# Performance work log

Hardware: AMD Instinct MI355X
Metric: run time of the kernel (lower is better)

Reference implementation:

```python
import jax, jax.numpy as jnp
import numpy as np

BN_EPS = 1e-5


def setup_inputs() -> dict:
    key = jax.random.key(0)
    ks = jax.random.split(key, 16)
    N, E, IN, H, A, L = 50000, 400000, 128, 192, 192, 3
    s = 0.02
    inp = {
        "x": jax.random.normal(ks[0], (N, IN), dtype=jnp.float32),
        "edge_index": jax.random.randint(ks[1], (2, E), 0, N, dtype=jnp.int32),
        "seed_idx": 123,
        "proj_w": jax.random.normal(ks[2], (IN, H), dtype=jnp.float32) * s,
        "proj_b": jnp.zeros((H,), dtype=jnp.float32),
        "mlp1_w": jax.random.normal(ks[3], (L, H, H), dtype=jnp.float32) * s,
        "mlp1_b": jnp.zeros((L, H), dtype=jnp.float32),
        "mlp2_w": jax.random.normal(ks[4], (L, H, H), dtype=jnp.float32) * s,
        "mlp2_b": jnp.zeros((L, H), dtype=jnp.float32),
        "eps": jnp.zeros((L,), dtype=jnp.float32),  # GIN train_eps init 0
        "bn_g": jnp.ones((L, H), dtype=jnp.float32),
        "bn_b": jnp.zeros((L, H), dtype=jnp.float32),
        "W1": jax.random.normal(ks[5], (H, A), dtype=jnp.float32) * s,
        "W2": jax.random.normal(ks[6], (H, A), dtype=jnp.float32) * s,
        "w_attn": jax.random.normal(ks[7], (A,), dtype=jnp.float32) * s,
        "cls_w": jax.random.normal(ks[8], (H,), dtype=jnp.float32) * s,
        "cls_b": jnp.zeros((1,), dtype=jnp.float32),
    }
    return inp


def _forward(x, edge_index, seed_idx, proj_w, proj_b, mlp1_w, mlp1_b,
             mlp2_w, mlp2_b, eps, bn_g, bn_b, W1, W2, w_attn, cls_w, cls_b):
    N = x.shape[0]
    src, dst = edge_index[0], edge_index[1]
    h = jax.nn.relu(x @ proj_w + proj_b)  # [N, H]
    L = mlp1_w.shape[0]
    for l in range(L):
        # GINConv: mlp((1+eps)*h + sum_{j->i} h_j) via scatter-add on dst
        agg = jax.ops.segment_sum(h[src], dst, num_segments=N)  # [N, H]
        z = (1.0 + eps[l]) * h + agg
        z = jax.nn.relu(z @ mlp1_w[l] + mlp1_b[l]) @ mlp2_w[l] + mlp2_b[l]
        # BatchNorm over nodes (batch statistics)
        mu = z.mean(axis=0)
        var = z.var(axis=0)
        z = (z - mu) * jax.lax.rsqrt(var + BN_EPS) * bn_g[l] + bn_b[l]
        h = jax.nn.relu(z)  # dropout is identity in eval
    h_seed = h[seed_idx]  # valid seed index branch
    zat = jnp.tanh(h @ W1 + h_seed @ W2)          # [N, A]
    e = jax.nn.leaky_relu(zat @ w_attn, 0.2)      # [N]
    alpha = jax.nn.softmax(e, axis=0)             # [N]
    readout = alpha @ h                           # [H]
    logit = readout @ cls_w + cls_b               # [1]
    return logit, alpha


def reference(x, edge_index, seed_idx, proj_w, proj_b, mlp1_w, mlp1_b,
              mlp2_w, mlp2_b, eps, bn_g, bn_b, W1, W2, w_attn, cls_w, cls_b):
    return _forward(x, edge_index, seed_idx, proj_w, proj_b, mlp1_w, mlp1_b,
                    mlp2_w, mlp2_b, eps, bn_g, bn_b, W1, W2, w_attn, cls_w, cls_b)
```

## Files before the change

kernel.cpp:

```cpp
#include <hip/hip_runtime.h>
#include <hip/hip_bf16.h>

#define N_NODES 50000
#define N_EDGES 400000
#define DIM_IN  128
#define DIM_H   192
#define N_LAYERS 3
#define BN_EPSF 1e-5f
#define SCAN_NBLK 49
#define INV_N (1.f / N_NODES)
#define NSHADOW 8
#define SSTRIDE 384

typedef __attribute__((ext_vector_type(8))) short short8;
typedef __attribute__((ext_vector_type(4))) float floatx4;

union FragU { uint4 u; short8 s; };

__device__ __forceinline__ float relu_f(float x) { return x > 0.f ? x : 0.f; }
__device__ __forceinline__ unsigned short f2bf(float x) {
  __hip_bfloat16 h = __float2bfloat16(x);
  return *reinterpret_cast<unsigned short*>(&h);
}
__device__ __forceinline__ float bf2f(unsigned short b) {
  return __uint_as_float(((unsigned)b) << 16);
}
__device__ __forceinline__ float bflo(unsigned u) { return __uint_as_float(u << 16); }
__device__ __forceinline__ float bfhi(unsigned u) { return __uint_as_float(u & 0xffff0000u); }

__global__ void k_hist(const int* __restrict__ edge, int* __restrict__ cnt) {
  int e = blockIdx.x * 256 + threadIdx.x;
  if (e < N_EDGES) atomicAdd(&cnt[edge[N_EDGES + e]], 1);
}

__global__ void k_scanA(const int* __restrict__ deg, int* __restrict__ part, int* __restrict__ bsum) {
  __shared__ int buf[1024];
  int g = blockIdx.x * 1024 + threadIdx.x;
  int v = (g < N_NODES) ? deg[g] : 0;
  buf[threadIdx.x] = v;
  __syncthreads();
  for (int off = 1; off < 1024; off <<= 1) {
    int t = (threadIdx.x >= off) ? buf[threadIdx.x - off] : 0;
    __syncthreads();
    buf[threadIdx.x] += t;
    __syncthreads();
  }
  if (g < N_NODES) part[g] = buf[threadIdx.x];
  if (threadIdx.x == 1023) bsum[blockIdx.x] = buf[1023];
}

__global__ void k_scanB(int* __restrict__ bsum) {
  __shared__ int b[64];
  int t = threadIdx.x;
  b[t] = (t < SCAN_NBLK) ? bsum[t] : 0;
  __syncthreads();
  for (int off = 1; off < 64; off <<= 1) {
    int v = (t >= off) ? b[t - off] : 0;
    __syncthreads();
    b[t] += v;
    __syncthreads();
  }
  if (t < SCAN_NBLK) bsum[t] = t ? b[t - 1] : 0;
}

__global__ void k_scanC(const int* __restrict__ part, const int* __restrict__ bsum,
                        int* __restrict__ rowptr, int* __restrict__ cursor) {
  int g = blockIdx.x * 256 + threadIdx.x;
  if (g == 0) { rowptr[0] = 0; cursor[0] = 0; }
  if (g < N_NODES) {
    int v = part[g] + bsum[g >> 10];
    rowptr[g + 1] = v;
    if (g + 1 < N_NODES) cursor[g + 1] = v;
  }
}

__global__ void k_fill(const int* __restrict__ edge, int* __restrict__ cursor, int* __restrict__ csr) {
  int e = blockIdx.x * 256 + threadIdx.x;
  if (e < N_EDGES) {
    int s = edge[e];
    int d = edge[N_EDGES + e];
    int pos = atomicAdd(&cursor[d], 1);
    csr[pos] = s;
  }
}

__global__ void k_wtp(const float* __restrict__ m1, const float* __restrict__ m2,
                      const float* __restrict__ wa, const float* __restrict__ pw,
                      uint4* __restrict__ outp) {
  const int NH = 7 * 24 * 192;
  const int NP = 16 * 192;
  int idx = blockIdx.x * 256 + threadIdx.x;
  if (idx >= NH + NP) return;
  union { uint4 u; unsigned short h[8]; } fr;
  if (idx < NH) {
    int mat = idx / (24 * 192);
    int rem = idx - mat * (24 * 192);
    int kidx = rem / 192, col = rem - kidx * 192;
    const float* src = mat < 3 ? m1 + (size_t)mat * (DIM_H * DIM_H)
                     : (mat < 6 ? m2 + (size_t)(mat - 3) * (DIM_H * DIM_H) : wa);
#pragma unroll
    for (int t = 0; t < 8; ++t) fr.h[t] = f2bf(src[(size_t)(kidx * 8 + t) * DIM_H + col]);
  } else {
    int rem = idx - NH;
    int kidx = rem / 192, col = rem - kidx * 192;
#pragma unroll
    for (int t = 0; t < 8; ++t) fr.h[t] = f2bf(pw[(size_t)(kidx * 8 + t) * DIM_H + col]);
  }
  outp[idx] = fr.u;
}

template <bool BN>
__global__ void k_agg(const unsigned short* __restrict__ z, const int* __restrict__ rowptr,
                      const int* __restrict__ csr, const float* __restrict__ stats,
                      const float* __restrict__ bng, const float* __restrict__ bnb,
                      const float* __restrict__ eps, int l, unsigned short* __restrict__ outA) {
  int wid = threadIdx.x >> 6, lane = threadIdx.x & 63;
  int node = blockIdx.x * 4 + wid;
  if (node >= N_NODES || lane >= 48) return;
  int c = lane * 4;
  float4 sc4 = {1.f, 1.f, 1.f, 1.f}, sh4 = {0.f, 0.f, 0.f, 0.f};
  if (BN) {
    float4 st = {0.f, 0.f, 0.f, 0.f}, sq = {0.f, 0.f, 0.f, 0.f};
#pragma unroll
    for (int g = 0; g < NSHADOW; ++g) {
      const float* sp = stats + g * SSTRIDE;
      float4 a = *(const float4*)(sp + c);
      float4 b = *(const float4*)(sp + DIM_H + c);
      st.x += a.x; st.y += a.y; st.z += a.z; st.w += a.w;
      sq.x += b.x; sq.y += b.y; sq.z += b.z; sq.w += b.w;
    }
    float4 g4 = *(const float4*)(bng + c);
    float4 b4 = *(const float4*)(bnb + c);
    float mu, rs;
    mu = st.x * INV_N; rs = rsqrtf(sq.x * INV_N - mu * mu + BN_EPSF); sc4.x = g4.x * rs; sh4.x = b4.x - mu * sc4.x;
    mu = st.y * INV_N; rs = rsqrtf(sq.y * INV_N - mu * mu + BN_EPSF); sc4.y = g4.y * rs; sh4.y = b4.y - mu * sc4.y;
    mu = st.z * INV_N; rs = rsqrtf(sq.z * INV_N - mu * mu + BN_EPSF); sc4.z = g4.z * rs; sh4.z = b4.z - mu * sc4.z;
    mu = st.w * INV_N; rs = rsqrtf(sq.w * INV_N - mu * mu + BN_EPSF); sc4.w = g4.w * rs; sh4.w = b4.w - mu * sc4.w;
  }
  float a0 = 0.f, a1 = 0.f, a2 = 0.f, a3 = 0.f;
  int beg = rowptr[node], end = rowptr[node + 1];
#define ACCU(U)                                                          \
  {                                                                      \
    float v0 = bflo((U).x), v1 = bfhi((U).x);                            \
    float v2 = bflo((U).y), v3 = bfhi((U).y);                            \
    if (BN) {                                                            \
      v0 = relu_f(v0 * sc4.x + sh4.x);                                   \
      v1 = relu_f(v1 * sc4.y + sh4.y);                                   \
      v2 = relu_f(v2 * sc4.z + sh4.z);                                   \
      v3 = relu_f(v3 * sc4.w + sh4.w);                                   \
    }                                                                    \
    a0 += v0; a1 += v1; a2 += v2; a3 += v3;                              \
  }
  int j = beg;
  for (; j + 4 <= end; j += 4) {
    int s0 = csr[j], s1 = csr[j + 1], s2 = csr[j + 2], s3 = csr[j + 3];
    uint2 u0 = *(const uint2*)(z + (size_t)s0 * DIM_H + c);
    uint2 u1 = *(const uint2*)(z + (size_t)s1 * DIM_H + c);
    uint2 u2 = *(const uint2*)(z + (size_t)s2 * DIM_H + c);
    uint2 u3 = *(const uint2*)(z + (size_t)s3 * DIM_H + c);
    ACCU(u0) ACCU(u1) ACCU(u2) ACCU(u3)
  }
  for (; j < end; ++j) {
    int s0 = csr[j];
    uint2 u0 = *(const uint2*)(z + (size_t)s0 * DIM_H + c);
    ACCU(u0)
  }
#undef ACCU
  float ep = 1.f + eps[l];
  uint2 us = *(const uint2*)(z + (size_t)node * DIM_H + c);
  {
    float v0 = bflo(us.x), v1 = bfhi(us.x), v2 = bflo(us.y), v3 = bfhi(us.y);
    if (BN) {
      v0 = relu_f(v0 * sc4.x + sh4.x);
      v1 = relu_f(v1 * sc4.y + sh4.y);
      v2 = relu_f(v2 * sc4.z + sh4.z);
      v3 = relu_f(v3 * sc4.w + sh4.w);
    }
    a0 += ep * v0; a1 += ep * v1; a2 += ep * v2; a3 += ep * v3;
  }
  uint2 o;
  o.x = (unsigned)f2bf(a0) | ((unsigned)f2bf(a1) << 16);
  o.y = (unsigned)f2bf(a2) | ((unsigned)f2bf(a3) << 16);
  *(uint2*)(outA + (size_t)node * DIM_H + c) = o;
}

template <int KS>
__device__ __forceinline__ void load_b(const uint4* __restrict__ Bp, int colbase, int kq, int lr,
                                       FragU (&b)[KS][3]) {
#pragma unroll
  for (int ks = 0; ks < KS; ++ks)
#pragma unroll
    for (int n = 0; n < 3; ++n)
      b[ks][n].u = Bp[(ks * 4 + kq) * 192 + colbase + n * 16 + lr];
}

template <int KS, int MT>
__device__ __forceinline__ void mfma_stage_pre(const uint4* a_lds, const FragU (&b)[KS][3],
                                               int kq, int lr, floatx4 (&acc)[MT][3]) {
#pragma unroll
  for (int ks = 0; ks < KS; ++ks) {
    int kidx = ks * 4 + kq;
    FragU a[MT];
#pragma unroll
    for (int m = 0; m < MT; ++m) a[m].u = a_lds[kidx * (MT * 16) + m * 16 + lr];
#pragma unroll
    for (int n = 0; n < 3; ++n)
#pragma unroll
      for (int m = 0; m < MT; ++m)
        acc[m][n] = __builtin_amdgcn_mfma_f32_16x16x32_bf16(a[m].s, b[ks][n].s, acc[m][n], 0, 0, 0);
  }
}

__global__ __launch_bounds__(256) void k_proj(const float* __restrict__ A,
                                              const uint4* __restrict__ Bp,
                                              const float* __restrict__ bias,
                                              unsigned short* __restrict__ C) {
  __shared__ uint4 a_lds[16 * 64];
  const int tid = threadIdx.x;
  const int rbase = blockIdx.x * 64;
  const int lane = tid & 63, w = tid >> 6;
  const int kq = lane >> 4, lr = lane & 15;
  const int colbase = w * 48;
  FragU b[4][3];
  load_b<4>(Bp, colbase, kq, lr, b);
#pragma unroll
  for (int i = 0; i < 4; ++i) {
    int row = tid >> 2, kidx = i * 4 + (tid & 3);
    int gr = rbase + row;
    gr = gr < N_NODES ? gr : N_NODES - 1;
    const float* ap = A + (size_t)gr * DIM_IN + kidx * 8;
    float4 v0 = *(const float4*)ap;
    float4 v1 = *(const float4*)(ap + 4);
    union { uint4 u; unsigned short h[8]; } fr;
    fr.h[0] = f2bf(v0.x); fr.h[1] = f2bf(v0.y); fr.h[2] = f2bf(v0.z); fr.h[3] = f2bf(v0.w);
    fr.h[4] = f2bf(v1.x); fr.h[5] = f2bf(v1.y); fr.h[6] = f2bf(v1.z); fr.h[7] = f2bf(v1.w);
    a_lds[kidx * 64 + row] = fr.u;
  }
  __syncthreads();
  floatx4 acc[4][3];
  floatx4 zero4 = {0.f, 0.f, 0.f, 0.f};
#pragma unroll
  for (int m = 0; m < 4; ++m)
#pragma unroll
    for (int n = 0; n < 3; ++n) acc[m][n] = zero4;
  mfma_stage_pre<4, 4>(a_lds, b, kq, lr, acc);
#pragma unroll
  for (int n = 0; n < 3; ++n) {
    int col = colbase + n * 16 + lr;
    float bb = bias[col];
#pragma unroll
    for (int m = 0; m < 4; ++m)
#pragma unroll
      for (int j = 0; j < 4; ++j) {
        int row = rbase + m * 16 + kq * 4 + j;
        if (row < N_NODES) C[(size_t)row * DIM_H + col] = f2bf(relu_f(acc[m][n][j] + bb));
      }
  }
}

__device__ __forceinline__ void z_epi(floatx4 (&acc)[2][3], unsigned short* zl, const float* __restrict__ b1,
                                      int colbase, int kq, int lr) {
#pragma unroll
  for (int n = 0; n < 3; ++n) {
    int col = colbase + n * 16 + lr;
    float bb = b1[col];
#pragma unroll
    for (int m = 0; m < 2; ++m)
#pragma unroll
      for (int j = 0; j < 4; ++j) {
        int rowl = m * 16 + kq * 4 + j;
        zl[(col >> 3) * 256 + rowl * 8 + (col & 7)] = f2bf(relu_f(acc[m][n][j] + bb));
      }
  }
}

__device__ __forceinline__ void out_epi(floatx4 (&acc)[2][3], unsigned short* __restrict__ Z,
                                        const float* __restrict__ b2, int rb, int colbase, int kq, int lr,
                                        float (&s3)[3], float (&q3)[3]) {
#pragma unroll
  for (int n = 0; n < 3; ++n) {
    int col = colbase + n * 16 + lr;
    float bb = b2[col];
#pragma unroll
    for (int m = 0; m < 2; ++m)
#pragma unroll
      for (int j = 0; j < 4; ++j) {
        int row = rb + m * 16 + kq * 4 + j;
        if (row < N_NODES) {
          float v = acc[m][n][j] + bb;
          Z[(size_t)row * DIM_H + col] = f2bf(v);
          s3[n] += v;
          q3[n] += v * v;
        }
      }
  }
}

__global__ __launch_bounds__(256, 3) void k_mlp(const unsigned short* __restrict__ A,
                                                const uint4* __restrict__ B1p, const float* __restrict__ b1,
                                                const uint4* __restrict__ B2p, const float* __restrict__ b2,
                                                unsigned short* __restrict__ Z, float* __restrict__ stats) {
  __shared__ uint4 a_lds[2][24 * 32];
  const int tid = threadIdx.x;
  const int rbase = blockIdx.x * 64;
  const int lane = tid & 63, w = tid >> 6;
  const int kq = lane >> 4, lr = lane & 15;
  const int colbase = w * 48;
  uint4 areg[2][3];
  const int arow = tid >> 3;
#pragma unroll
  for (int t = 0; t < 2; ++t) {
    int agr = rbase + t * 32 + arow;
    agr = agr < N_NODES ? agr : N_NODES - 1;
#pragma unroll
    for (int i = 0; i < 3; ++i) {
      int kidx = i * 8 + (tid & 7);
      areg[t][i] = *(const uint4*)(A + (size_t)agr * DIM_H + kidx * 8);
    }
  }
  FragU b1r[6][3];
  load_b<6>(B1p, colbase, kq, lr, b1r);
#pragma unroll
  for (int t = 0; t < 2; ++t)
#pragma unroll
    for (int i = 0; i < 3; ++i) {
      int kidx = i * 8 + (tid & 7);
      a_lds[t][kidx * 32 + arow] = areg[t][i];
    }
  __syncthreads();
  floatx4 zero4 = {0.f, 0.f, 0.f, 0.f};
  floatx4 acc0[2][3], acc1[2][3];
#pragma unroll
  for (int m = 0; m < 2; ++m)
#pragma unroll
    for (int n = 0; n < 3; ++n) { acc0[m][n] = zero4; acc1[m][n] = zero4; }
  mfma_stage_pre<6, 2>(a_lds[0], b1r, kq, lr, acc0);
  mfma_stage_pre<6, 2>(a_lds[1], b1r, kq, lr, acc1);
  FragU b2r[6][3];
  load_b<6>(B2p, colbase, kq, lr, b2r);
  __syncthreads();
  z_epi(acc0, (unsigned short*)a_lds[0], b1, colbase, kq, lr);
  z_epi(acc1, (unsigned short*)a_lds[1], b1, colbase, kq, lr);
  __syncthreads();
#pragma unroll
  for (int m = 0; m < 2; ++m)
#pragma unroll
    for (int n = 0; n < 3; ++n) { acc0[m][n] = zero4; acc1[m][n] = zero4; }
  mfma_stage_pre<6, 2>(a_lds[0], b2r, kq, lr, acc0);
  mfma_stage_pre<6, 2>(a_lds[1], b2r, kq, lr, acc1);
  float s3[3] = {0.f, 0.f, 0.f}, q3[3] = {0.f, 0.f, 0.f};
  out_epi(acc0, Z, b2, rbase, colbase, kq, lr, s3, q3);
  out_epi(acc1, Z, b2, rbase + 32, colbase, kq, lr, s3, q3);
  __syncthreads();
  float* ps = (float*)a_lds;
  float* pq = ps + DIM_H * 4;
#pragma unroll
  for (int n = 0; n < 3; ++n) {
    int col = colbase + n * 16 + lr;
    ps[col * 4 + kq] = s3[n];
    pq[col * 4 + kq] = q3[n];
  }
  __syncthreads();
  if (tid < DIM_H) {
    float ts = 0.f, tq = 0.f;
#pragma unroll
    for (int g = 0; g < 4; ++g) {
      ts += ps[tid * 4 + g];
      tq += pq[tid * 4 + g];
    }
    float* sp = stats + (blockIdx.x & (NSHADOW - 1)) * SSTRIDE;
    atomicAdd(&sp[tid], ts);
    atomicAdd(&sp[DIM_H + tid], tq);
  }
}

__global__ void k_seed_s2(const unsigned short* __restrict__ Zin, const float* __restrict__ stats,
                          const float* __restrict__ bng, const float* __restrict__ bnb,
                          const int* __restrict__ seedp, const float* __restrict__ W2,
                          float* __restrict__ s2) {
  __shared__ float hs[DIM_H];
  __shared__ float red[4][DIM_H];
  int tid = threadIdx.x;
  if (tid < DIM_H) {
    int seed = seedp[0];
    float ts = 0.f, tq = 0.f;
#pragma unroll
    for (int g = 0; g < NSHADOW; ++g) {
      ts += stats[g * SSTRIDE + tid];
      tq += stats[g * SSTRIDE + DIM_H + tid];
    }
    float mu = ts * INV_N;
    float rs = rsqrtf(tq * INV_N - mu * mu + BN_EPSF);
    float sc = bng[tid] * rs;
    float sh = bnb[tid] - mu * sc;
    hs[tid] = relu_f(bf2f(Zin[(size_t)seed * DIM_H + tid]) * sc + sh);
  }
  __syncthreads();
  int a = tid % DIM_H, grp = tid / DIM_H;
  float s = 0.f;
  for (int k = grp * 48; k < grp * 48 + 48; ++k) s = fmaf(hs[k], W2[(size_t)k * DIM_H + a], s);
  red[grp][a] = s;
  __syncthreads();
  if (tid < DIM_H) s2[tid] = red[0][tid] + red[1][tid] + red[2][tid] + red[3][tid];
}

__global__ __launch_bounds__(256, 3) void k_attnm(const unsigned short* __restrict__ Zin,
                                                  const float* __restrict__ stats,
                                                  const float* __restrict__ bng,
                                                  const float* __restrict__ bnb,
                                                  const uint4* __restrict__ Bp,
                                                  const float* __restrict__ s2,
                                                  const float* __restrict__ wat,
                                                  float* __restrict__ p, float* __restrict__ scal) {
  __shared__ uint4 a_lds[24 * 64];
  __shared__ float cs[DIM_H], ch[DIM_H];
  const int tid = threadIdx.x;
  const int rbase = blockIdx.x * 64;
  const int lane = tid & 63, w = tid >> 6;
  const int kq = lane >> 4, lr = lane & 15;
  const int colbase = w * 48;
  FragU b[6][3];
  load_b<6>(Bp, colbase, kq, lr, b);
  if (tid < DIM_H) {
    float ts = 0.f, tq = 0.f;
#pragma unroll
    for (int g = 0; g < NSHADOW; ++g) {
      ts += stats[g * SSTRIDE + tid];
      tq += stats[g * SSTRIDE + DIM_H + tid];
    }
    float mu = ts * INV_N;
    float rs = rsqrtf(tq * INV_N - mu * mu + BN_EPSF);
    float sc = bng[tid] * rs;
    cs[tid] = sc;
    ch[tid] = bnb[tid] - mu * sc;
  }
  __syncthreads();
#pragma unroll
  for (int i = 0; i < 6; ++i) {
    int row = tid >> 2, kidx = i * 4 + (tid & 3);
    int gr = rbase + row;
    gr = gr < N_NODES ? gr : N_NODES - 1;
    union { uint4 u; unsigned short h[8]; } v, o;
    v.u = *(const uint4*)(Zin + (size_t)gr * DIM_H + kidx * 8);
#pragma unroll
    for (int t = 0; t < 8; ++t)
      o.h[t] = f2bf(relu_f(bf2f(v.h[t]) * cs[kidx * 8 + t] + ch[kidx * 8 + t]));
    a_lds[kidx * 64 + row] = o.u;
  }
  __syncthreads();
  floatx4 zero4 = {0.f, 0.f, 0.f, 0.f};
  floatx4 acc[4][3];
#pragma unroll
  for (int m = 0; m < 4; ++m)
#pragma unroll
    for (int n = 0; n < 3; ++n) acc[m][n] = zero4;
  mfma_stage_pre<6, 4>(a_lds, b, kq, lr, acc);
  float pv[16];
#pragma unroll
  for (int t = 0; t < 16; ++t) pv[t] = 0.f;
#pragma unroll
  for (int n = 0; n < 3; ++n) {
    int col = colbase + n * 16 + lr;
    float s2c = s2[col];
    float wv = wat[col];
#pragma unroll
    for (int m = 0; m < 4; ++m)
#pragma unroll
      for (int j = 0; j < 4; ++j) {
        float xv = acc[m][n][j] + s2c;
        xv = fminf(fmaxf(xv, -10.f), 10.f);
        float t = __expf(2.f * xv);
        pv[m * 4 + j] = fmaf((t - 1.f) / (t + 1.f), wv, pv[m * 4 + j]);
      }
  }
  __syncthreads();
  float* part = (float*)a_lds;
#pragma unroll
  for (int m = 0; m < 4; ++m)
#pragma unroll
    for (int j = 0; j < 4; ++j)
      part[(m * 16 + kq * 4 + j) * 65 + w * 16 + lr] = pv[m * 4 + j];
  __syncthreads();
  if (tid < 64) {
    float s = 0.f;
#pragma unroll
    for (int i = 0; i < 64; ++i) s += part[tid * 65 + i];
    s = s > 0.f ? s : 0.2f * s;
    float pe = __expf(s);
    int gr = rbase + tid;
    bool valid = gr < N_NODES;
    if (valid) p[gr] = pe;
    pe = valid ? pe : 0.f;
#pragma unroll
    for (int off = 32; off > 0; off >>= 1) pe += __shfl_xor(pe, off);
    if (tid == 0) atomicAdd(&scal[0], pe);
  }
}

__global__ void k_alpha(const float* __restrict__ p, const float* __restrict__ scal,
                        float* __restrict__ alpha) {
  int i = blockIdx.x * 256 + threadIdx.x;
  if (i < N_NODES) alpha[i] = p[i] * (1.f / scal[0]);
}

#define RD_BLOCKS 512
__global__ __launch_bounds__(256) void k_readout(const float* __restrict__ p,
                                                 const unsigned short* __restrict__ Zin,
                                                 const float* __restrict__ stats,
                                                 const float* __restrict__ bng,
                                                 const float* __restrict__ bnb,
                                                 float* __restrict__ rdout) {
  __shared__ float red[4][DIM_H];
  const int tid = threadIdx.x;
  const int w = tid >> 6, lane = tid & 63;
  const int rpb = (N_NODES + RD_BLOCKS - 1) / RD_BLOCKS;
  int rbeg = blockIdx.x * rpb;
  int rend = rbeg + rpb;
  rend = rend < N_NODES ? rend : N_NODES;
  float a0 = 0.f, a1 = 0.f, a2 = 0.f, a3 = 0.f;
  if (lane < 48) {
    int c = lane * 4;
    float4 st = {0.f, 0.f, 0.f, 0.f}, sq = {0.f, 0.f, 0.f, 0.f};
#pragma unroll
    for (int g = 0; g < NSHADOW; ++g) {
      const float* sp = stats + g * SSTRIDE;
      float4 a = *(const float4*)(sp + c);
      float4 b = *(const float4*)(sp + DIM_H + c);
      st.x += a.x; st.y += a.y; st.z += a.z; st.w += a.w;
      sq.x += b.x; sq.y += b.y; sq.z += b.z; sq.w += b.w;
    }
    float4 g4 = *(const float4*)(bng + c);
    float4 b4 = *(const float4*)(bnb + c);
    float4 sc4, sh4;
    float mu, rs;
    mu = st.x * INV_N; rs = rsqrtf(sq.x * INV_N - mu * mu + BN_EPSF); sc4.x = g4.x * rs; sh4.x = b4.x - mu * sc4.x;
    mu = st.y * INV_N; rs = rsqrtf(sq.y * INV_N - mu * mu + BN_EPSF); sc4.y = g4.y * rs; sh4.y = b4.y - mu * sc4.y;
    mu = st.z * INV_N; rs = rsqrtf(sq.z * INV_N - mu * mu + BN_EPSF); sc4.z = g4.z * rs; sh4.z = b4.z - mu * sc4.z;
    mu = st.w * INV_N; rs = rsqrtf(sq.w * INV_N - mu * mu + BN_EPSF); sc4.w = g4.w * rs; sh4.w = b4.w - mu * sc4.w;
#pragma unroll 2
    for (int r = rbeg + w; r < rend; r += 4) {
      float pw = p[r];
      uint2 u = *(const uint2*)(Zin + (size_t)r * DIM_H + c);
      float v0 = relu_f(bflo(u.x) * sc4.x + sh4.x);
      float v1 = relu_f(bfhi(u.x) * sc4.y + sh4.y);
      float v2 = relu_f(bflo(u.y) * sc4.z + sh4.z);
      float v3 = relu_f(bfhi(u.y) * sc4.w + sh4.w);
      a0 = fmaf(pw, v0, a0); a1 = fmaf(pw, v1, a1);
      a2 = fmaf(pw, v2, a2); a3 = fmaf(pw, v3, a3);
    }
    float4 o = {a0, a1, a2, a3};
    *(float4*)&red[w][c] = o;
  }
  __syncthreads();
  if (tid < DIM_H) {
    float s = red[0][tid] + red[1][tid] + red[2][tid] + red[3][tid];
    atomicAdd(&rdout[tid], s);
  }
}

__global__ void k_logit(const float* __restrict__ rdout, const float* __restrict__ scal,
                        const float* __restrict__ cw, const float* __restrict__ cb,
                        float* __restrict__ out) {
  __shared__ float buf[256];
  int tid = threadIdx.x;
  buf[tid] = (tid < DIM_H) ? rdout[tid] * cw[tid] : 0.f;
  __syncthreads();
  for (int s = 128; s > 0; s >>= 1) {
    if (tid < s) buf[tid] += buf[tid + s];
    __syncthreads();
  }
  if (tid == 0) out[0] = buf[0] * (1.f / scal[0]) + cb[0];
}

extern "C" void kernel_launch(void* const* d_in, const int* in_sizes, int n_in,
                              void* d_out, int out_size, void* d_ws, size_t ws_size,
                              hipStream_t stream) {
  const float* x      = (const float*)d_in[0];
  const int*   edge   = (const int*)d_in[1];
  const int*   seedp  = (const int*)d_in[2];
  const float* proj_w = (const float*)d_in[3];
  const float* proj_b = (const float*)d_in[4];
  const float* mlp1_w = (const float*)d_in[5];
  const float* mlp1_b = (const float*)d_in[6];
  const float* mlp2_w = (const float*)d_in[7];
  const float* mlp2_b = (const float*)d_in[8];
  const float* eps    = (const float*)d_in[9];
  const float* bn_g   = (const float*)d_in[10];
  const float* bn_b   = (const float*)d_in[11];
  const float* W1     = (const float*)d_in[12];
  const float* W2     = (const float*)d_in[13];
  const float* w_attn = (const float*)d_in[14];
  const float* cls_w  = (const float*)d_in[15];
  const float* cls_b  = (const float*)d_in[16];
  float* out = (float*)d_out;

  char* ws = (char*)d_ws;
  size_t off = 0;
  auto alloc = [&](size_t bytes) -> void* {
    void* p = ws + off;
    off = (off + bytes + 255) & ~(size_t)255;
    return p;
  };
  unsigned short* buf0 = (unsigned short*)alloc((size_t)N_NODES * DIM_H * 2);
  unsigned short* buf1 = (unsigned short*)alloc((size_t)N_NODES * DIM_H * 2);
  float* pbuf   = (float*)alloc((size_t)N_NODES * 4);
  int* rowptr   = (int*)alloc((size_t)(N_NODES + 1) * 4);
  int* cursor   = (int*)alloc((size_t)(N_NODES + 1) * 4);
  int* csr      = (int*)alloc((size_t)N_EDGES * 4);
  int* part     = (int*)alloc((size_t)N_NODES * 4);
  int* bsum     = (int*)alloc(64 * 4);
  float* stats  = (float*)alloc((size_t)NSHADOW * SSTRIDE * 4);
  float* s2     = (float*)alloc(DIM_H * 4);
  float* scalrd = (float*)alloc(256 * 4);
  float* scal   = scalrd;
  float* rdout  = scalrd + 64;
  uint4* WTall  = (uint4*)alloc((size_t)(7 * 24 * 192 + 16 * 192) * 16);

  const uint4* B1p[N_LAYERS] = {WTall, WTall + 4608, WTall + 2 * 4608};
  const uint4* B2p[N_LAYERS] = {WTall + 3 * 4608, WTall + 4 * 4608, WTall + 5 * 4608};
  const uint4* Bap = WTall + 6 * 4608;
  const uint4* Bpp = WTall + 7 * 4608;

  const int GRID64 = (N_NODES + 63) / 64;

  k_wtp<<<(7 * 24 * 192 + 16 * 192 + 255) / 256, 256, 0, stream>>>(mlp1_w, mlp2_w, W1, proj_w, WTall);

  hipMemsetAsync(cursor, 0, (size_t)(N_NODES + 1) * 4, stream);
  k_hist<<<(N_EDGES + 255) / 256, 256, 0, stream>>>(edge, cursor);
  k_scanA<<<SCAN_NBLK, 1024, 0, stream>>>(cursor, part, bsum);
  k_scanB<<<1, 64, 0, stream>>>(bsum);
  k_scanC<<<(N_NODES + 255) / 256, 256, 0, stream>>>(part, bsum, rowptr, cursor);
  k_fill<<<(N_EDGES + 255) / 256, 256, 0, stream>>>(edge, cursor, csr);

  k_proj<<<GRID64, 256, 0, stream>>>(x, Bpp, proj_b, buf0);

  unsigned short* cur = buf0;
  unsigned short* nxt = buf1;
  for (int l = 0; l < N_LAYERS; ++l) {
    const float* g_prev = bn_g + (size_t)(l - 1) * DIM_H;
    const float* b_prev = bn_b + (size_t)(l - 1) * DIM_H;
    if (l == 0)
      k_agg<false><<<(N_NODES + 3) / 4, 256, 0, stream>>>(cur, rowptr, csr, stats, g_prev, b_prev, eps, l, nxt);
    else
      k_agg<true><<<(N_NODES + 3) / 4, 256, 0, stream>>>(cur, rowptr, csr, stats, g_prev, b_prev, eps, l, nxt);
    hipMemsetAsync(stats, 0, (size_t)NSHADOW * SSTRIDE * 4, stream);
    k_mlp<<<GRID64, 256, 0, stream>>>(nxt, B1p[l], mlp1_b + (size_t)l * DIM_H,
                                      B2p[l], mlp2_b + (size_t)l * DIM_H, nxt, stats);
    unsigned short* t = cur; cur = nxt; nxt = t;
  }
  const float* g2 = bn_g + (size_t)2 * DIM_H;
  const float* b2c = bn_b + (size_t)2 * DIM_H;

  hipMemsetAsync(scalrd, 0, 256 * 4, stream);
  k_seed_s2<<<1, 768, 0, stream>>>(cur, stats, g2, b2c, seedp, W2, s2);
  k_attnm<<<GRID64, 256, 0, stream>>>(cur, stats, g2, b2c, Bap, s2, w_attn, pbuf, scal);
  k_alpha<<<(N_NODES + 255) / 256, 256, 0, stream>>>(pbuf, scal, out + 1);
  k_readout<<<RD_BLOCKS, 256, 0, stream>>>(pbuf, cur, stats, g2, b2c, rdout);
  k_logit<<<1, 256, 0, stream>>>(rdout, scal, cls_w, cls_b, out);
}
```

Measured before the change: 338.6 us.

## Split GIN aggregation into 32-column chunks with LDS-staged CSR per node block

Replaces the one-wave-per-node gather with blocks that each own 128 nodes and one 32-column (64-byte) slice of the feature dimension. Each block stages its rowptr and CSR neighbour lists in shared memory. Sixteen lanes cover one node, so a wave processes four nodes at once, and the blockIdx mapping orders the chunks so concurrently resident blocks hit a narrower column slice of the gathered features, aiming for better L2 locality. The cost is that neighbour indices are loaded and read redundantly across six chunk-blocks, the gathers are narrower (4 bytes per lane), and lanes sit idle under divergent degrees within a wave.

```diff
diff --git a/kernel.cpp b/kernel.cpp
--- a/kernel.cpp
+++ b/kernel.cpp
@@ -11,6 +11,8 @@
 #define INV_N (1.f / N_NODES)
 #define NSHADOW 8
 #define SSTRIDE 384
+#define AG_NPB 128
+#define AG_CAP 3072
 
 typedef __attribute__((ext_vector_type(8))) short short8;
 typedef __attribute__((ext_vector_type(4))) float floatx4;
@@ -110,78 +112,107 @@
 }
 
 template <bool BN>
-__global__ void k_agg(const unsigned short* __restrict__ z, const int* __restrict__ rowptr,
-                      const int* __restrict__ csr, const float* __restrict__ stats,
-                      const float* __restrict__ bng, const float* __restrict__ bnb,
-                      const float* __restrict__ eps, int l, unsigned short* __restrict__ outA) {
-  int wid = threadIdx.x >> 6, lane = threadIdx.x & 63;
-  int node = blockIdx.x * 4 + wid;
-  if (node >= N_NODES || lane >= 48) return;
-  int c = lane * 4;
-  float4 sc4 = {1.f, 1.f, 1.f, 1.f}, sh4 = {0.f, 0.f, 0.f, 0.f};
-  if (BN) {
-    float4 st = {0.f, 0.f, 0.f, 0.f}, sq = {0.f, 0.f, 0.f, 0.f};
-#pragma unroll
-    for (int g = 0; g < NSHADOW; ++g) {
-      const float* sp = stats + g * SSTRIDE;
-      float4 a = *(const float4*)(sp + c);
-      float4 b = *(const float4*)(sp + DIM_H + c);
-      st.x += a.x; st.y += a.y; st.z += a.z; st.w += a.w;
-      sq.x += b.x; sq.y += b.y; sq.z += b.z; sq.w += b.w;
-    }
-    float4 g4 = *(const float4*)(bng + c);
-    float4 b4 = *(const float4*)(bnb + c);
-    float mu, rs;
-    mu = st.x * INV_N; rs = rsqrtf(sq.x * INV_N - mu * mu + BN_EPSF); sc4.x = g4.x * rs; sh4.x = b4.x - mu * sc4.x;
-    mu = st.y * INV_N; rs = rsqrtf(sq.y * INV_N - mu * mu + BN_EPSF); sc4.y = g4.y * rs; sh4.y = b4.y - mu * sc4.y;
-    mu = st.z * INV_N; rs = rsqrtf(sq.z * INV_N - mu * mu + BN_EPSF); sc4.z = g4.z * rs; sh4.z = b4.z - mu * sc4.z;
-    mu = st.w * INV_N; rs = rsqrtf(sq.w * INV_N - mu * mu + BN_EPSF); sc4.w = g4.w * rs; sh4.w = b4.w - mu * sc4.w;
-  }
-  float a0 = 0.f, a1 = 0.f, a2 = 0.f, a3 = 0.f;
-  int beg = rowptr[node], end = rowptr[node + 1];
-#define ACCU(U)                                                          \
-  {                                                                      \
-    float v0 = bflo((U).x), v1 = bfhi((U).x);                            \
-    float v2 = bflo((U).y), v3 = bfhi((U).y);                            \
-    if (BN) {                                                            \
-      v0 = relu_f(v0 * sc4.x + sh4.x);                                   \
-      v1 = relu_f(v1 * sc4.y + sh4.y);                                   \
-      v2 = relu_f(v2 * sc4.z + sh4.z);                                   \
-      v3 = relu_f(v3 * sc4.w + sh4.w);                                   \
-    }                                                                    \
-    a0 += v0; a1 += v1; a2 += v2; a3 += v3;                              \
-  }
-  int j = beg;
-  for (; j + 4 <= end; j += 4) {
-    int s0 = csr[j], s1 = csr[j + 1], s2 = csr[j + 2], s3 = csr[j + 3];
-    uint2 u0 = *(const uint2*)(z + (size_t)s0 * DIM_H + c);
-    uint2 u1 = *(const uint2*)(z + (size_t)s1 * DIM_H + c);
-    uint2 u2 = *(const uint2*)(z + (size_t)s2 * DIM_H + c);
-    uint2 u3 = *(const uint2*)(z + (size_t)s3 * DIM_H + c);
-    ACCU(u0) ACCU(u1) ACCU(u2) ACCU(u3)
-  }
-  for (; j < end; ++j) {
-    int s0 = csr[j];
-    uint2 u0 = *(const uint2*)(z + (size_t)s0 * DIM_H + c);
-    ACCU(u0)
-  }
-#undef ACCU
-  float ep = 1.f + eps[l];
-  uint2 us = *(const uint2*)(z + (size_t)node * DIM_H + c);
-  {
-    float v0 = bflo(us.x), v1 = bfhi(us.x), v2 = bflo(us.y), v3 = bfhi(us.y);
+__global__ __launch_bounds__(256) void k_aggc(
+    const unsigned short* __restrict__ z, const int* __restrict__ rowptr,
+    const int* __restrict__ csr, const float* __restrict__ stats,
+    const float* __restrict__ bng, const float* __restrict__ bnb,
+    const float* __restrict__ eps, int l, unsigned short* __restrict__ outA,
+    int NBH, int NB) {
+  __shared__ int rp[AG_NPB + 1];
+  __shared__ int sCsr[AG_CAP];
+  __shared__ float csh[64];
+  const int tid = threadIdx.x;
+  const int lq = blockIdx.x & 7;
+  const int idx8 = blockIdx.x >> 3;
+  int chunk, nb;
+  if (lq < 6) {
+    chunk = lq; nb = idx8;
+    if (lq < 2 && nb >= NBH) return;
+  } else {
+    chunk = lq - 6; nb = NBH + idx8;
+    if (nb >= NB) return;
+  }
+  const int node0 = nb * AG_NPB;
+  const int cb = chunk * 32;
+  if (tid < 32) {
+    float scv = 1.f, shv = 0.f;
     if (BN) {
-      v0 = relu_f(v0 * sc4.x + sh4.x);
-      v1 = relu_f(v1 * sc4.y + sh4.y);
-      v2 = relu_f(v2 * sc4.z + sh4.z);
-      v3 = relu_f(v3 * sc4.w + sh4.w);
-    }
-    a0 += ep * v0; a1 += ep * v1; a2 += ep * v2; a3 += ep * v3;
-  }
-  uint2 o;
-  o.x = (unsigned)f2bf(a0) | ((unsigned)f2bf(a1) << 16);
-  o.y = (unsigned)f2bf(a2) | ((unsigned)f2bf(a3) << 16);
-  *(uint2*)(outA + (size_t)node * DIM_H + c) = o;
+      int c = cb + tid;
+      float ts = 0.f, tq = 0.f;
+#pragma unroll
+      for (int g = 0; g < NSHADOW; ++g) {
+        ts += stats[g * SSTRIDE + c];
+        tq += stats[g * SSTRIDE + DIM_H + c];
+      }
+      float mu = ts * INV_N;
+      float rs = rsqrtf(tq * INV_N - mu * mu + BN_EPSF);
+      scv = bng[c] * rs;
+      shv = bnb[c] - mu * scv;
+    }
+    csh[tid] = scv; csh[32 + tid] = shv;
+  }
+  for (int i = tid; i <= AG_NPB; i += 256) {
+    int n = node0 + i;
+    rp[i] = rowptr[n < N_NODES ? n : N_NODES];
+  }
+  __syncthreads();
+  const int e0 = rp[0];
+  const int cnt = rp[AG_NPB] - e0;
+  const bool fits = (cnt <= AG_CAP);
+  const int* csrp;
+  int cbeg, clampHi;
+  if (fits) {
+    for (int i = tid; i < cnt; i += 256) sCsr[i] = csr[e0 + i];
+    csrp = sCsr; cbeg = e0; clampHi = cnt > 0 ? cnt - 1 : 0;
+  } else {
+    csrp = csr; cbeg = 0; clampHi = N_EDGES - 1;
+  }
+  __syncthreads();
+  const int w = tid >> 6, lane = tid & 63;
+  const int g = lane >> 4, cl = lane & 15;
+  const float sc0 = csh[cl * 2], sc1 = csh[cl * 2 + 1];
+  const float sh0 = csh[32 + cl * 2], sh1 = csh[32 + cl * 2 + 1];
+  const float ep = 1.f + eps[l];
+  const unsigned laneByte = (unsigned)(cb + cl * 2) * 2;
+  const char* zb = (const char*)z;
+#pragma unroll
+  for (int it = 0; it < AG_NPB / 16; ++it) {
+    int li = w * (AG_NPB / 4) + it * 4 + g;
+    int n = node0 + li;
+    int beg = rp[li] - cbeg, end = rp[li + 1] - cbeg;
+    int deg = end - beg;
+    float a0 = 0.f, a1 = 0.f;
+    int j = 0;
+    while (__any(j < deg)) {
+      {
+        bool act = j < deg;
+        int idx = beg + j; idx = idx < clampHi ? idx : clampHi;
+        int s = csrp[idx];
+        unsigned u = *(const unsigned*)(zb + (((unsigned)(s * 3)) << 7) + laneByte);
+        float v0 = bflo(u), v1 = bfhi(u);
+        if (BN) { v0 = relu_f(fmaf(v0, sc0, sh0)); v1 = relu_f(fmaf(v1, sc1, sh1)); }
+        a0 += act ? v0 : 0.f; a1 += act ? v1 : 0.f;
+      }
+      {
+        bool act = j + 1 < deg;
+        int idx = beg + j + 1; idx = idx < clampHi ? idx : clampHi;
+        int s = csrp[idx];
+        unsigned u = *(const unsigned*)(zb + (((unsigned)(s * 3)) << 7) + laneByte);
+        float v0 = bflo(u), v1 = bfhi(u);
+        if (BN) { v0 = relu_f(fmaf(v0, sc0, sh0)); v1 = relu_f(fmaf(v1, sc1, sh1)); }
+        a0 += act ? v0 : 0.f; a1 += act ? v1 : 0.f;
+      }
+      j += 2;
+    }
+    if (n < N_NODES) {
+      unsigned u = *(const unsigned*)(zb + (((unsigned)(n * 3)) << 7) + laneByte);
+      float v0 = bflo(u), v1 = bfhi(u);
+      if (BN) { v0 = relu_f(fmaf(v0, sc0, sh0)); v1 = relu_f(fmaf(v1, sc1, sh1)); }
+      a0 += ep * v0; a1 += ep * v1;
+      unsigned o = (unsigned)f2bf(a0) | ((unsigned)f2bf(a1) << 16);
+      *(unsigned*)((char*)outA + (((unsigned)(n * 3)) << 7) + laneByte) = o;
+    }
+  }
 }
 
 template <int KS>
@@ -622,6 +653,8 @@
   const uint4* Bpp = WTall + 7 * 4608;
 
   const int GRID64 = (N_NODES + 63) / 64;
+  const int NB = (N_NODES + AG_NPB - 1) / AG_NPB;
+  const int NBH = (NB + 1) / 2;
 
   k_wtp<<<(7 * 24 * 192 + 16 * 192 + 255) / 256, 256, 0, stream>>>(mlp1_w, mlp2_w, W1, proj_w, WTall);
 
@@ -640,9 +673,9 @@
     const float* g_prev = bn_g + (size_t)(l - 1) * DIM_H;
     const float* b_prev = bn_b + (size_t)(l - 1) * DIM_H;
     if (l == 0)
-      k_agg<false><<<(N_NODES + 3) / 4, 256, 0, stream>>>(cur, rowptr, csr, stats, g_prev, b_prev, eps, l, nxt);
+      k_aggc<false><<<8 * NB, 256, 0, stream>>>(cur, rowptr, csr, stats, g_prev, b_prev, eps, l, nxt, NBH, NB);
     else
-      k_agg<true><<<(N_NODES + 3) / 4, 256, 0, stream>>>(cur, rowptr, csr, stats, g_prev, b_prev, eps, l, nxt);
+      k_aggc<true><<<8 * NB, 256, 0, stream>>>(cur, rowptr, csr, stats, g_prev, b_prev, eps, l, nxt, NBH, NB);
     hipMemsetAsync(stats, 0, (size_t)NSHADOW * SSTRIDE * 4, stream);
     k_mlp<<<GRID64, 256, 0, stream>>>(nxt, B1p[l], mlp1_b + (size_t)l * DIM_H,
                                       B2p[l], mlp2_b + (size_t)l * DIM_H, nxt, stats);
```

Result: slower. 387.4 us (+14.4%).
